# Kernel optimization log

Hardware: AMD Instinct MI355X
Metric: run time of the kernel (lower is better)

## Reference

```python
import jax, jax.numpy as jnp
import numpy as np


def log_g(x):
    # log of g(x) = where(x>=0, x+0.5, sigmoid(x))
    return jnp.where(x >= 0, jnp.log(jax.nn.relu(x) + 0.5), -jax.nn.softplus(-x))


def heinsen_associative_scan_log(log_coeffs, log_values):
    a_star = jnp.cumsum(log_coeffs, axis=1)
    log_h0_plus_b_star = jax.lax.cumlogsumexp(log_values - a_star, axis=1)
    return jnp.exp(a_star + log_h0_plus_b_star)


def setup_inputs() -> dict:
    key = jax.random.key(0)
    k1, k2 = jax.random.split(key)
    B, T, D = 4, 8192, 512
    x = jax.random.normal(k1, (B, T, D), dtype=jnp.float32)
    # Linear(dim, 2*dim, bias=False); scaled like torch default init
    W = jax.random.normal(k2, (D, 2 * D), dtype=jnp.float32) * (1.0 / np.sqrt(D))
    return {"x": x, "W": W}


def reference(x, W):
    hg = jnp.einsum('btd,de->bte', x, W)  # [B,T,2D]
    hidden, gate = jnp.split(hg, 2, axis=-1)
    log_z = -jax.nn.softplus(-gate)       # log sigmoid(gate)
    log_coeffs = -jax.nn.softplus(gate)   # log (1 - sigmoid(gate))
    log_tilde_h = log_g(hidden)
    out = heinsen_associative_scan_log(log_coeffs, log_z + log_tilde_h)
    return out
```

## Files before the change

kernel.cpp:

```cpp
#include <hip/hip_runtime.h>

typedef unsigned short u16;
typedef unsigned int   u32;

typedef __bf16 bf16x8 __attribute__((ext_vector_type(8)));
typedef float  f32x4  __attribute__((ext_vector_type(4)));

#define B_DIM 4
#define T_DIM 8192
#define D_DIM 512
#define M_DIM (B_DIM * T_DIM)
#define K_DIM D_DIM
#define NC    256
#define LCH   32

__device__ __forceinline__ u16 f2bf(float f) {
  u32 u = __float_as_uint(f);
  u32 r = (u + 0x7FFFu + ((u >> 16) & 1u)) >> 16;
  return (u16)r;
}
__device__ __forceinline__ float bf2f(u16 b) {
  return __uint_as_float(((u32)b) << 16);
}

__device__ __forceinline__ void gload_lds16(const u16* g, u16* lds) {
  __builtin_amdgcn_global_load_lds(
      (const __attribute__((address_space(1))) void*)g,
      (__attribute__((address_space(3))) void*)lds, 16, 0, 0);
}


__global__ void convert_x(const float4* __restrict__ in, u16* __restrict__ out, int n4) {
  int i = blockIdx.x * blockDim.x + threadIdx.x;
  int stride = gridDim.x * blockDim.x;
  for (; i < n4; i += stride) {
    float4 f = in[i];
    u32 w0 = (u32)f2bf(f.x) | ((u32)f2bf(f.y) << 16);
    u32 w1 = (u32)f2bf(f.z) | ((u32)f2bf(f.w) << 16);
    *reinterpret_cast<uint2*>(out + (size_t)i * 4) = make_uint2(w0, w1);
  }
}

__global__ void convert_wt(const float* __restrict__ W, u16* __restrict__ wt) {
  int idx = blockIdx.x * blockDim.x + threadIdx.x;
  int n  = idx & 1023;
  int k0 = (idx >> 10) * 8;
  float f[8];
#pragma unroll
  for (int j = 0; j < 8; ++j) f[j] = W[(size_t)(k0 + j) * 1024 + n];
  u32 w[4];
#pragma unroll
  for (int j = 0; j < 4; ++j)
    w[j] = (u32)f2bf(f[2 * j]) | ((u32)f2bf(f[2 * j + 1]) << 16);
  *reinterpret_cast<uint4*>(wt + (size_t)n * 512 + k0) = make_uint4(w[0], w[1], w[2], w[3]);
}


#define BK 64
#define NT (K_DIM / BK)

__global__ __launch_bounds__(256) void gemm_act(const u16* __restrict__ xb,
                                                const u16* __restrict__ wt,
                                                u32* __restrict__ av_buf,
                                                float* __restrict__ Asum,
                                                float* __restrict__ Bsum) {
  __shared__ u16 As[2][128 * BK];
  __shared__ u16 Bs[2][128 * BK];

  const int tid  = threadIdx.x;
  const int lane = tid & 63;
  const int wave = tid >> 6;
  const int l15  = lane & 15;
  const int lh   = lane >> 4;
  const int wr   = wave >> 1;
  const int wc   = wave & 1;
  const int m_base = blockIdx.x * 128;
  const int d0     = blockIdx.y * 64;

  const int srow = tid >> 3;
  const int sk   = (((tid & 7) ^ (srow & 7)) << 3);

  int garow[4], gnrow[4];
#pragma unroll
  for (int i = 0; i < 4; ++i) {
    garow[i] = m_base + i * 32 + srow;
    gnrow[i] = ((i & 1) ? 512 : 0) + d0 + ((i >> 1) << 5) + srow;
  }
  const int lds_w = wave * 512;

  f32x4 acc[4][4];
#pragma unroll
  for (int m = 0; m < 4; ++m)
#pragma unroll
    for (int n = 0; n < 4; ++n)
      acc[m][n] = (f32x4){0.f, 0.f, 0.f, 0.f};

#define STAGE(buf, kofs)                                                        \
  do {                                                                          \
    _Pragma("unroll")                                                           \
    for (int i = 0; i < 4; ++i) {                                               \
      gload_lds16(xb + (size_t)garow[i] * K_DIM + (kofs) + sk,                  \
                  &As[buf][i * 2048 + lds_w]);                                  \
      gload_lds16(wt + (size_t)gnrow[i] * K_DIM + (kofs) + sk,                  \
                  &Bs[buf][i * 2048 + lds_w]);                                  \
    }                                                                           \
  } while (0)

  STAGE(0, 0);
  int cur = 0;
  for (int t = 0; t < NT; ++t) {
    __syncthreads();
    if (t + 1 < NT) STAGE(cur ^ 1, (t + 1) * BK);
#pragma unroll
    for (int kk = 0; kk < 2; ++kk) {
      bf16x8 af[4], bfr[4];
#pragma unroll
      for (int m = 0; m < 4; ++m) {
        int r = 64 * wr + m * 16 + l15;
        int slot = (4 * kk + lh) ^ (l15 & 7);
        af[m] = *reinterpret_cast<const bf16x8*>(&As[cur][r * 64 + slot * 8]);
      }
#pragma unroll
      for (int n = 0; n < 4; ++n) {
        int r = 64 * wc + n * 16 + l15;
        int slot = (4 * kk + lh) ^ (l15 & 7);
        bfr[n] = *reinterpret_cast<const bf16x8*>(&Bs[cur][r * 64 + slot * 8]);
      }
#pragma unroll
      for (int m = 0; m < 4; ++m)
#pragma unroll
        for (int n = 0; n < 4; ++n)
          acc[m][n] = __builtin_amdgcn_mfma_f32_16x16x32_bf16(af[m], bfr[n], acc[m][n], 0, 0, 0);
    }
    cur ^= 1;
  }
#undef STAGE

  const int row_w = m_base + 64 * wr;
#pragma unroll
  for (int h = 0; h < 2; ++h) {
    float Ar[2][2], Br[2][2];
#pragma unroll
    for (int mm = 0; mm < 2; ++mm) {
      const int m = 2 * h + mm;
#pragma unroll
      for (int n = 0; n < 2; ++n) {
        float A = 1.f, Bv = 0.f;
        const int dch = d0 + 32 * wc + 16 * n + l15;
#pragma unroll
        for (int r = 0; r < 4; ++r) {
          float hid = acc[m][n][r];
          float gt  = acc[m][n + 2][r];
          float e   = __expf(gt);
          float inv = 1.f / (1.f + e);
          float g   = (hid >= 0.f) ? (hid + 0.5f) : (1.f / (1.f + __expf(-hid)));
          float v   = (e * inv) * g;
          u16 abf = f2bf(inv);
          u16 vbf = f2bf(v);
          const int grow = row_w + 16 * m + 4 * lh + r;
          av_buf[(size_t)grow * D_DIM + dch] = (u32)abf | ((u32)vbf << 16);
          float af = bf2f(abf), vf = bf2f(vbf);
          Bv = af * Bv + vf;
          A *= af;
        }
        Ar[n][mm] = A; Br[n][mm] = Bv;
      }
    }
#pragma unroll
    for (int n = 0; n < 2; ++n)
#pragma unroll
      for (int mm = 0; mm < 2; ++mm) {
        float A = Ar[n][mm], Bv = Br[n][mm];
#pragma unroll
        for (int d = 1; d <= 2; d <<= 1) {
          float pA = __shfl(A, lane - 16 * d);
          float pB = __shfl(Bv, lane - 16 * d);
          if (lh >= d) { Bv = A * pB + Bv; A = A * pA; }
        }
        Ar[n][mm] = A; Br[n][mm] = Bv;
      }
    if (lh == 3) {
      const int grow = row_w + 32 * h;
      const int b = grow >> 13;
      const int c = (grow & 8191) >> 5;
      const size_t o = ((size_t)(b * NC + c)) * D_DIM;
#pragma unroll
      for (int n = 0; n < 2; ++n) {
        const int dch = d0 + 32 * wc + 16 * n + l15;
        float Ac = Ar[n][0] * Ar[n][1];
        float Bc = Ar[n][1] * Br[n][0] + Br[n][1];
        Asum[o + dch] = Ac;
        Bsum[o + dch] = Bc;
      }
    }
  }
}


__global__ __launch_bounds__(256) void scan_pass2(const float* __restrict__ Asum,
                                                  const float* __restrict__ Bsum,
                                                  float* __restrict__ carry) {
  int idx = blockIdx.x * blockDim.x + threadIdx.x;
  int b = idx >> 9;
  int d = idx & 511;
  float h = 0.f;
  for (int c = 0; c < NC; ++c) {
    size_t o = ((size_t)(b * NC + c)) * D_DIM + d;
    carry[o] = h;
    h = Asum[o] * h + Bsum[o];
  }
}


__global__ __launch_bounds__(128) void scan_pass3(const u32* __restrict__ av_buf,
                                                  const float4* __restrict__ carry,
                                                  float4* __restrict__ out) {
  const int c = blockIdx.x;
  const int b = blockIdx.y;
  const int d4 = threadIdx.x;
  float4 hh = carry[((size_t)(b * NC + c)) * 128 + d4];
  float h[4] = {hh.x, hh.y, hh.z, hh.w};
  size_t base = ((size_t)b * T_DIM + (size_t)c * LCH) * D_DIM + d4 * 4;
  for (int t = 0; t < LCH; ++t) {
    uint4 w = *reinterpret_cast<const uint4*>(av_buf + base);
    h[0] = bf2f(w.x & 0xffff) * h[0] + bf2f(w.x >> 16);
    h[1] = bf2f(w.y & 0xffff) * h[1] + bf2f(w.y >> 16);
    h[2] = bf2f(w.z & 0xffff) * h[2] + bf2f(w.z >> 16);
    h[3] = bf2f(w.w & 0xffff) * h[3] + bf2f(w.w >> 16);
    out[base >> 2] = make_float4(h[0], h[1], h[2], h[3]);
    base += D_DIM;
  }
}


extern "C" void kernel_launch(void* const* d_in, const int* in_sizes, int n_in,
                              void* d_out, int out_size, void* d_ws, size_t ws_size,
                              hipStream_t stream) {
  const float* x = (const float*)d_in[0];
  const float* W = (const float*)d_in[1];
  float* out = (float*)d_out;

  char* ws = (char*)d_ws;
  u16*   xb     = (u16*)(ws + 0);
  u16*   wtp    = (u16*)(ws + 33554432);
  u32*   av_buf = (u32*)(ws + 34603008);
  float* Asum   = (float*)(ws + 101711872);
  float* Bsum   = (float*)(ws + 103809024);
  float* carry  = (float*)(ws + 105906176);
  if (ws_size < 108003328ULL) return;

  convert_x<<<2048, 256, 0, stream>>>((const float4*)x, xb, (M_DIM * K_DIM) / 4);
  convert_wt<<<256, 256, 0, stream>>>(W, wtp);
  gemm_act<<<dim3(M_DIM / 128, D_DIM / 64), 256, 0, stream>>>(xb, wtp, av_buf, Asum, Bsum);
  scan_pass2<<<8, 256, 0, stream>>>(Asum, Bsum, carry);
  scan_pass3<<<dim3(NC, B_DIM), 128, 0, stream>>>(av_buf, (const float4*)carry, (float4*)out);
}
```

Before: 121.3 us.

## Deepen GEMM LDS pipeline to four stages with smaller K tiles

The GEMM main loop now uses K tiles of 32 instead of 64 and a 4-buffer ring of LDS stages with three loads in flight. Waits use explicit vmcnt counts instead of a full __syncthreads. A new swizzled layout packs two rows per 64-element LDS line. The goal is to hide global-to-LDS load latency behind MFMA work. In exchange there are twice as many barriers per K and hand-counted waitcnt values that must match the issued loads.

```diff
diff --git a/kernel.cpp b/kernel.cpp
--- a/kernel.cpp
+++ b/kernel.cpp
@@ -56,16 +56,16 @@
 }
 
 
-#define BK 64
-#define NT (K_DIM / BK)
+#define BK 32
+#define NT 16
 
 __global__ __launch_bounds__(256) void gemm_act(const u16* __restrict__ xb,
                                                 const u16* __restrict__ wt,
                                                 u32* __restrict__ av_buf,
                                                 float* __restrict__ Asum,
                                                 float* __restrict__ Bsum) {
-  __shared__ u16 As[2][128 * BK];
-  __shared__ u16 Bs[2][128 * BK];
+  __shared__ u16 As[4][4096];
+  __shared__ u16 Bs[4][4096];
 
   const int tid  = threadIdx.x;
   const int lane = tid & 63;
@@ -77,16 +77,15 @@
   const int m_base = blockIdx.x * 128;
   const int d0     = blockIdx.y * 64;
 
-  const int srow = tid >> 3;
-  const int sk   = (((tid & 7) ^ (srow & 7)) << 3);
-
-  int garow[4], gnrow[4];
-#pragma unroll
-  for (int i = 0; i < 4; ++i) {
-    garow[i] = m_base + i * 32 + srow;
-    gnrow[i] = ((i & 1) ? 512 : 0) + d0 + ((i >> 1) << 5) + srow;
-  }
-  const int lds_w = wave * 512;
+  const int pair0 = tid >> 3;
+  const int s3    = (tid & 7) ^ (pair0 & 7);
+  const int lrow0 = (pair0 << 1) | (s3 >> 2);
+  const int scol  = (s3 & 3) << 3;
+  const int garow0 = m_base + lrow0;
+  const int garow1 = garow0 + 64;
+  const int gn0 = ((lrow0 >> 5) ? 512 : 0) + d0 + (lrow0 & 31);
+  const int gn1 = gn0 + 32;
+  const int ldsw = wave * 512;
 
   f32x4 acc[4][4];
 #pragma unroll
@@ -95,46 +94,55 @@
     for (int n = 0; n < 4; ++n)
       acc[m][n] = (f32x4){0.f, 0.f, 0.f, 0.f};
 
-#define STAGE(buf, kofs)                                                        \
-  do {                                                                          \
-    _Pragma("unroll")                                                           \
-    for (int i = 0; i < 4; ++i) {                                               \
-      gload_lds16(xb + (size_t)garow[i] * K_DIM + (kofs) + sk,                  \
-                  &As[buf][i * 2048 + lds_w]);                                  \
-      gload_lds16(wt + (size_t)gnrow[i] * K_DIM + (kofs) + sk,                  \
-                  &Bs[buf][i * 2048 + lds_w]);                                  \
-    }                                                                           \
+#define STAGE(buf, kt)                                                      \
+  do {                                                                      \
+    const int ko = (kt) * BK + scol;                                        \
+    gload_lds16(xb + (size_t)garow0 * K_DIM + ko, &As[buf][ldsw]);          \
+    gload_lds16(xb + (size_t)garow1 * K_DIM + ko, &As[buf][2048 + ldsw]);   \
+    gload_lds16(wt + (size_t)gn0 * K_DIM + ko, &Bs[buf][ldsw]);             \
+    gload_lds16(wt + (size_t)gn1 * K_DIM + ko, &Bs[buf][2048 + ldsw]);      \
   } while (0)
 
+#define AOFF(row) (((row) >> 1) * 64 + (((((((row) & 1) << 2) | lh)) ^ (((row) >> 1) & 7)) << 3))
+
+#define COMPUTE(cur)                                                        \
+  do {                                                                      \
+    bf16x8 af[4], bfr[4];                                                   \
+    _Pragma("unroll")                                                       \
+    for (int m = 0; m < 4; ++m)                                             \
+      af[m] = *reinterpret_cast<const bf16x8*>(&As[cur][AOFF(64 * wr + 16 * m + l15)]); \
+    _Pragma("unroll")                                                       \
+    for (int n = 0; n < 4; ++n)                                             \
+      bfr[n] = *reinterpret_cast<const bf16x8*>(&Bs[cur][AOFF(64 * wc + 16 * n + l15)]); \
+    _Pragma("unroll")                                                       \
+    for (int m = 0; m < 4; ++m)                                             \
+      _Pragma("unroll")                                                     \
+      for (int n = 0; n < 4; ++n)                                           \
+        acc[m][n] = __builtin_amdgcn_mfma_f32_16x16x32_bf16(af[m], bfr[n], acc[m][n], 0, 0, 0); \
+  } while (0)
+
+#define WAITBAR(N)                                                          \
+  do {                                                                      \
+    asm volatile("s_waitcnt vmcnt(" #N ")" ::: "memory");                   \
+    __builtin_amdgcn_sched_barrier(0);                                      \
+    __builtin_amdgcn_s_barrier();                                           \
+    __builtin_amdgcn_sched_barrier(0);                                      \
+  } while (0)
+
   STAGE(0, 0);
-  int cur = 0;
-  for (int t = 0; t < NT; ++t) {
-    __syncthreads();
-    if (t + 1 < NT) STAGE(cur ^ 1, (t + 1) * BK);
-#pragma unroll
-    for (int kk = 0; kk < 2; ++kk) {
-      bf16x8 af[4], bfr[4];
-#pragma unroll
-      for (int m = 0; m < 4; ++m) {
-        int r = 64 * wr + m * 16 + l15;
-        int slot = (4 * kk + lh) ^ (l15 & 7);
-        af[m] = *reinterpret_cast<const bf16x8*>(&As[cur][r * 64 + slot * 8]);
-      }
-#pragma unroll
-      for (int n = 0; n < 4; ++n) {
-        int r = 64 * wc + n * 16 + l15;
-        int slot = (4 * kk + lh) ^ (l15 & 7);
-        bfr[n] = *reinterpret_cast<const bf16x8*>(&Bs[cur][r * 64 + slot * 8]);
-      }
-#pragma unroll
-      for (int m = 0; m < 4; ++m)
-#pragma unroll
-        for (int n = 0; n < 4; ++n)
-          acc[m][n] = __builtin_amdgcn_mfma_f32_16x16x32_bf16(af[m], bfr[n], acc[m][n], 0, 0, 0);
-    }
-    cur ^= 1;
-  }
+  STAGE(1, 1);
+  STAGE(2, 2);
+  for (int t = 0; t < 13; ++t) {
+    WAITBAR(8);
+    STAGE((t + 3) & 3, t + 3);
+    COMPUTE(t & 3);
+  }
+  WAITBAR(8);  COMPUTE(1);
+  WAITBAR(4);  COMPUTE(2);
+  WAITBAR(0);  COMPUTE(3);
 #undef STAGE
+#undef COMPUTE
+#undef WAITBAR
 
   const int row_w = m_base + 64 * wr;
 #pragma unroll
```

After: 124.7 us. 1.03x slower.
